# Optimization experiments

Hardware: AMD Instinct MI355X
Metric: run time of the kernel (lower is better)

The kernel has to match this reference:

```python
import jax, jax.numpy as jnp
import numpy as np

B, T_ENC, E, T_DEC, N_MELS, H, A = 32, 256, 512, 200, 80, 1024, 128


def setup_inputs() -> dict:
    key = jax.random.key(0)
    ks = jax.random.split(key, 20)
    rn = lambda k, s, sc: (jax.random.normal(k, s, jnp.float32) * sc)
    return {
        "inputs": rn(ks[0], (B, T_ENC, E), 1.0),
        "padded_mels": rn(ks[1], (B, N_MELS, T_DEC), 1.0),
        "W_enc": rn(ks[2], (E, A), 0.04),
        "W_q": rn(ks[3], (H, A), 0.03),
        "conv_w": rn(ks[4], (32, 1, 31), 0.18),
        "conv_b": jnp.zeros((32,), jnp.float32),
        "W_loc": rn(ks[5], (32, A), 0.18),
        "v_e": rn(ks[6], (A,), 0.09),
        "pw1": rn(ks[7], (N_MELS, 256), 0.11),
        "pb1": jnp.zeros((256,), jnp.float32),
        "pw2": rn(ks[8], (256, 256), 0.06),
        "pb2": jnp.zeros((256,), jnp.float32),
        "Wi1": rn(ks[9], (256 + E, 4 * H), 0.03),
        "Wh1": rn(ks[10], (H, 4 * H), 0.03),
        "bl1": jnp.zeros((4 * H,), jnp.float32),
        "Wi2": rn(ks[11], (H, 4 * H), 0.03),
        "Wh2": rn(ks[12], (H, 4 * H), 0.03),
        "bl2": jnp.zeros((4 * H,), jnp.float32),
        "Wp": rn(ks[13], (H + E, N_MELS), 0.025),
        "bp": jnp.zeros((N_MELS,), jnp.float32),
    }


def _lstm_cell(x, h, c, Wi, Wh, b):
    g = x @ Wi + h @ Wh + b
    i, f, gg, o = jnp.split(g, 4, axis=-1)
    c = jax.nn.sigmoid(f) * c + jax.nn.sigmoid(i) * jnp.tanh(gg)
    h = jax.nn.sigmoid(o) * jnp.tanh(c)
    return h, c


def reference(inputs, padded_mels, W_enc, W_q, conv_w, conv_b, W_loc, v_e,
              pw1, pb1, pw2, pb2, Wi1, Wh1, bl1, Wi2, Wh2, bl2, Wp, bp):
    b, t_enc, e = inputs.shape
    n_mels, t_dec = padded_mels.shape[1], padded_mels.shape[2]
    proc_enc = inputs @ W_enc  # [B, T_enc, A]
    # teacher forcing: prepend go frame, use frames 0..T_dec-1 as inputs
    go = jnp.zeros((b, n_mels, 1), inputs.dtype)
    prev_mels = jnp.moveaxis(jnp.concatenate([go, padded_mels], axis=-1)[:, :, :-1], -1, 0)  # [T_dec,B,80]

    def step(carry, prev_mel):
        h1, c1, h2, c2, ctx, aw_cum = carry
        # prenet (dropout omitted: eval/deterministic reference)
        x = jax.nn.relu(prev_mel @ pw1 + pb1)
        x = jax.nn.relu(x @ pw2 + pb2)
        # 2-layer LSTM on [prenet, prev context]
        lstm_in = jnp.concatenate([x, ctx], axis=-1)
        h1n, c1n = _lstm_cell(lstm_in, h1, c1, Wi1, Wh1, bl1)
        h2n, c2n = _lstm_cell(h1n, h2, c2, Wi2, Wh2, bl2)
        # location-sensitive attention
        q = h2n @ W_q  # [B, A]
        loc = jax.lax.conv_general_dilated(aw_cum[:, None, :], conv_w, (1,), "SAME",
                                           dimension_numbers=("NCH", "OIH", "NCH"))
        loc = loc + conv_b[None, :, None]
        loc = jnp.swapaxes(loc, 1, 2) @ W_loc  # [B, T_enc, A]
        energies = jnp.tanh(q[:, None, :] + loc + proc_enc) @ v_e  # [B, T_enc]
        aw = jax.nn.softmax(energies, axis=1)
        ctx_n = jnp.einsum("bt,bte->be", aw, inputs)
        out = jnp.concatenate([h2n, ctx_n], axis=-1) @ Wp + bp  # [B, 80]
        return (h1n, c1n, h2n, c2n, ctx_n, aw_cum + aw), out

    z = lambda *s: jnp.zeros(s, inputs.dtype)
    carry0 = (z(b, H), z(b, H), z(b, H), z(b, H), z(b, e), z(b, t_enc))
    _, mels = jax.lax.scan(step, carry0, prev_mels)
    return mels  # [T_dec, B, 80]
```

## Files before the change

kernel.cpp:

```cpp
#include <hip/hip_runtime.h>
#include <hip/hip_fp16.h>

#define BB   32
#define TENC 256
#define EE   512
#define TDEC 200
#define NM   80
#define HH   1024
#define AA   128
#define GG   4096
#define K1   1792
#define K2   2048

typedef _Float16 h8v  __attribute__((ext_vector_type(8)));
typedef float    f32x4 __attribute__((ext_vector_type(4)));

__device__ __forceinline__ float sigf(float x){ return 1.0f/(1.0f + __expf(-x)); }
__device__ __forceinline__ float tanhfast(float x){ return 1.0f - 2.0f/(1.0f + __expf(2.0f*x)); }


__global__ void k_zero(float* __restrict__ p, int n){
    int i = blockIdx.x*blockDim.x + threadIdx.x;
    if(i < n) p[i] = 0.f;
}

__global__ void k_cvt_half(const float* __restrict__ src, __half* __restrict__ dst, int n){
    int i = blockIdx.x*blockDim.x + threadIdx.x;
    int stride = gridDim.x*blockDim.x;
    for(; i<n; i+=stride) dst[i] = __float2half(src[i]);
}

__global__ __launch_bounds__(256) void k_transpose2(const float* __restrict__ src,
                                                    _Float16* __restrict__ dst,
                                                    int K, int C, int dstStride, int kOff, int pack){
    __shared__ float tile[32][33];
    const int tid = threadIdx.x;
    const int c0 = blockIdx.x*32, k0 = blockIdx.y*32;
    const int cl = tid & 31, r8 = tid >> 5;
    #pragma unroll
    for(int i=0;i<4;i++){
        const int k = k0 + r8 + i*8;
        if(k < K && c0+cl < C) tile[r8 + i*8][cl] = src[(size_t)k*C + c0 + cl];
    }
    __syncthreads();
    const int kl = tid & 31, c8 = tid >> 5;
    #pragma unroll
    for(int i=0;i<4;i++){
        const int c = c0 + c8 + i*8;
        if(c < C && k0+kl < K){
            const int p = pack ? ((c & 1023)*4 + (c >> 10)) : c;
            dst[(size_t)p*dstStride + kOff + k0 + kl] = (_Float16)tile[kl][c8 + i*8];
        }
    }
}

__global__ __launch_bounds__(256) void k_wfrag(const _Float16* __restrict__ WT,
                                               _Float16* __restrict__ WF, int K){
    const int tid = threadIdx.x;
    const int l = tid & 63, f = tid >> 6;
    const int ct = blockIdx.y;
    const int kc = blockIdx.x*4 + f;
    const h8v v = *(const h8v*)(WT + (size_t)(ct*16 + (l & 15))*K + kc*32 + ((l >> 4) << 3));
    *(h8v*)(WF + ((size_t)(ct*(K >> 5) + kc)*64 + l)*8) = v;
}

__global__ __launch_bounds__(128) void k_proc_enc(const float* __restrict__ inputs,
                                                  const float* __restrict__ Wenc,
                                                  __half* __restrict__ pe_h){
    const int row = blockIdx.x;
    const int a   = threadIdx.x;
    const float* in = inputs + (size_t)row*EE;
    float acc = 0.f;
    for(int k=0;k<EE;k++) acc = fmaf(in[k], Wenc[k*AA + a], acc);
    pe_h[(size_t)row*AA + a] = __float2half(acc);
}

__global__ __launch_bounds__(320) void k_pip(const float* __restrict__ inputs,
                                             const float* __restrict__ Wp_c,
                                             __half* __restrict__ PIP){
    const int b = blockIdx.x >> 6, t4 = (blockIdx.x & 63)*4;
    __shared__ float xs[4*EE];
    const int tid = threadIdx.x;
    for(int i=tid; i<4*EE; i+=320) xs[i] = inputs[((size_t)b*TENC + t4)*EE + i];
    __syncthreads();
    const int tl = tid/80, m = tid%80;
    float acc = 0.f;
    for(int k=0;k<EE;k++) acc = fmaf(xs[tl*EE + k], Wp_c[k*NM + m], acc);
    PIP[((size_t)b*TENC + t4 + tl)*NM + m] = __float2half(acc);
}

__global__ __launch_bounds__(256) void k_prenet(const float* __restrict__ pmels,
                                                const float* __restrict__ pw1, const float* __restrict__ pb1,
                                                const float* __restrict__ pw2, const float* __restrict__ pb2,
                                                _Float16* __restrict__ XS1h){
    const int t = blockIdx.x;
    __shared__ float pm[BB*NM];
    __shared__ float h1s[BB*256];
    const int tid = threadIdx.x;
    for(int el=tid; el<BB*NM; el+=256){
        const int b = el/NM, m = el%NM;
        pm[el] = (t==0) ? 0.f : pmels[(size_t)(b*NM + m)*TDEC + (t-1)];
    }
    __syncthreads();
    const int a = tid;
    float acc[BB];
    #pragma unroll
    for(int b=0;b<BB;b++) acc[b]=0.f;
    for(int m=0;m<NM;m++){
        const float w = pw1[m*256 + a];
        #pragma unroll
        for(int b=0;b<BB;b++) acc[b] = fmaf(pm[b*NM+m], w, acc[b]);
    }
    {
        const float bias = pb1[a];
        for(int b=0;b<BB;b++) h1s[b*256+a] = fmaxf(acc[b]+bias, 0.f);
    }
    __syncthreads();
    #pragma unroll
    for(int b=0;b<BB;b++) acc[b]=0.f;
    for(int k=0;k<256;k++){
        const float w = pw2[k*256 + a];
        #pragma unroll
        for(int b=0;b<BB;b++) acc[b] = fmaf(h1s[b*256+k], w, acc[b]);
    }
    {
        const float bias = pb2[a];
        #pragma unroll
        for(int b=0;b<BB;b++)
            XS1h[((size_t)t*BB + b)*K1 + a] = (_Float16)fmaxf(acc[b]+bias, 0.f);
    }
}

__global__ void k_mloc(const float* __restrict__ conv_w, const float* __restrict__ conv_b,
                       const float* __restrict__ W_loc, float* __restrict__ Mloc, float* __restrict__ cbp){
    const int a = threadIdx.x;
    for(int d=0; d<31; d++){
        float s = 0.f;
        for(int ch=0; ch<32; ch++) s = fmaf(conv_w[ch*31 + d], W_loc[ch*AA + a], s);
        Mloc[d*AA + a] = s;
    }
    float s = 0.f;
    for(int ch=0; ch<32; ch++) s = fmaf(conv_b[ch], W_loc[ch*AA + a], s);
    cbp[a] = s;
}


template<int K>
__global__ __launch_bounds__(512) void k_lstm_mfma(
    const _Float16* __restrict__ XSh, const _Float16* __restrict__ WF,
    const float* __restrict__ bias, float* __restrict__ cst,
    _Float16* __restrict__ hA, int strideA, int offA,
    _Float16* __restrict__ hB, int strideB, int offB,
    float* __restrict__ hF)
{
    constexpr int KCN = K/128;
    __shared__ float part[4*32*18];
    const int tid = threadIdx.x, bid = blockIdx.x;
    const int l = tid & 63, w = tid >> 6;
    const int kw = w & 3, mh = w >> 2;

    f32x4 acc0 = {0.f,0.f,0.f,0.f}, acc1 = {0.f,0.f,0.f,0.f};
    const int row = mh*16 + (l & 15);
    const _Float16* aptr = XSh + (size_t)row*K + kw*(K/4) + ((l >> 4) << 3);
    const _Float16* bptr = WF + ((size_t)(bid*(K >> 5) + kw*KCN)*64 + l)*8;
    #pragma unroll
    for(int kc=0; kc<KCN; kc+=2){
        const h8v a0 = *(const h8v*)(aptr + (size_t)kc*32);
        const h8v b0 = *(const h8v*)(bptr + (size_t)kc*512);
        const h8v a1 = *(const h8v*)(aptr + (size_t)(kc+1)*32);
        const h8v b1 = *(const h8v*)(bptr + (size_t)(kc+1)*512);
        acc0 = __builtin_amdgcn_mfma_f32_16x16x32_f16(a0, b0, acc0, 0, 0, 0);
        acc1 = __builtin_amdgcn_mfma_f32_16x16x32_f16(a1, b1, acc1, 0, 0, 0);
    }
    {
        const int r0 = mh*16 + ((l >> 4) << 2);
        const int c  = l & 15;
        #pragma unroll
        for(int j=0;j<4;j++)
            part[(kw*32 + r0 + j)*18 + c] = acc0[j] + acc1[j];
    }
    __syncthreads();
    if(tid < 128){
        const int b = tid & 31, cl = tid >> 5;
        float g[4];
        #pragma unroll
        for(int gi=0; gi<4; gi++){
            const int c = cl*4 + gi;
            float s = part[(0*32 + b)*18 + c] + part[(1*32 + b)*18 + c]
                    + part[(2*32 + b)*18 + c] + part[(3*32 + b)*18 + c];
            const int p = bid*16 + c;
            g[gi] = s + bias[(p & 3)*HH + (p >> 2)];
        }
        const int cell = bid*4 + cl;
        const int ci = cell*BB + b;
        const float cn = sigf(g[1])*cst[ci] + sigf(g[0])*tanhfast(g[2]);
        cst[ci] = cn;
        const float hv = sigf(g[3])*tanhfast(cn);
        hA[(size_t)b*strideA + offA + cell] = (_Float16)hv;
        if(hB) hB[(size_t)b*strideB + offB + cell] = (_Float16)hv;
        if(hF) hF[(size_t)b*HH + cell] = hv;
    }
}

__global__ __launch_bounds__(256) void k_qe(
    const float* __restrict__ h2f,
    const _Float16* __restrict__ WqT, const float* __restrict__ cbp,
    const float* __restrict__ Mloc, const float* __restrict__ ve,
    const float* __restrict__ awc, const __half* __restrict__ pe,
    float* __restrict__ e_ws)
{
    const int b = blockIdx.x >> 3, ts = blockIdx.x & 7;
    const int t0 = ts*32;
    const int tid = threadIdx.x;
    __shared__ float h2s[1024], qc[256], qf[128], ml[31*AA], ves[AA], awin[64], ep[256];
    for(int i=tid; i<1024; i+=256) h2s[i] = h2f[(size_t)b*HH + i];
    for(int i=tid; i<31*AA; i+=256) ml[i] = Mloc[i];
    if(tid < AA) ves[tid] = ve[tid];
    if(tid < 62){
        const int g = t0 - 15 + tid;
        awin[tid] = (g>=0 && g<TENC) ? awc[b*TENC+g] : 0.f;
    }
    __syncthreads();
    {
        const int a = tid & 127, tp = tid >> 7;
        float qa = 0.f;
        const _Float16* wq = WqT + (size_t)a*HH + tp*512;
        const float* hs = h2s + tp*512;
        for(int kb=0; kb<512; kb+=8){
            const h8v w8 = *(const h8v*)(wq + kb);
            #pragma unroll
            for(int i2=0;i2<8;i2++) qa = fmaf((float)w8[i2], hs[kb+i2], qa);
        }
        qc[tp*AA + a] = qa;
    }
    __syncthreads();
    if(tid < AA) qf[tid] = qc[tid] + qc[AA+tid] + cbp[tid];
    __syncthreads();
    {
        const int tl = tid & 31, aq = tid >> 5;
        const int a0 = aq*16;
        const int t  = t0 + tl;
        float s[16];
        const __half* pp = pe + ((size_t)(b*TENC + t))*AA + a0;
        #pragma unroll
        for(int j=0;j<16;j++) s[j] = qf[a0+j] + __half2float(pp[j]);
        for(int d=0;d<31;d++){
            const float w = awin[tl+d];
            #pragma unroll
            for(int j=0;j<16;j++) s[j] = fmaf(w, ml[d*AA + a0 + j], s[j]);
        }
        float es = 0.f;
        #pragma unroll
        for(int j=0;j<16;j++) es = fmaf(tanhfast(s[j]), ves[a0+j], es);
        ep[aq*32 + tl] = es;
    }
    __syncthreads();
    if(tid < 32){
        float e = 0.f;
        #pragma unroll
        for(int q=0;q<8;q++) e += ep[q*32 + tid];
        e_ws[b*TENC + t0 + tid] = e;
    }
}

__global__ __launch_bounds__(256) void k_attn(
    const float* __restrict__ e_ws, const __half* __restrict__ inputs_h,
    const __half* __restrict__ PIP, float* __restrict__ awc,
    _Float16* __restrict__ XS1hn,
    const float* __restrict__ h2f,
    const _Float16* __restrict__ WohT, const float* __restrict__ bp,
    float* __restrict__ out, int t)
{
    const int b = blockIdx.x, tid = threadIdx.x;
    __shared__ float aw[TENC], h2s[1024], red[320], sred[8];
    for(int i=tid; i<1024; i+=256) h2s[i] = h2f[(size_t)b*HH + i];
    const float e = e_ws[b*TENC + tid];
    float m = e;
    #pragma unroll
    for(int o=32;o>=1;o>>=1) m = fmaxf(m, __shfl_xor(m, o));
    if((tid&63)==0) sred[tid>>6] = m;
    __syncthreads();
    m = fmaxf(fmaxf(sred[0],sred[1]), fmaxf(sred[2],sred[3]));
    const float p = __expf(e - m);
    float sum = p;
    #pragma unroll
    for(int o=32;o>=1;o>>=1) sum += __shfl_xor(sum, o);
    if((tid&63)==0) sred[4+(tid>>6)] = sum;
    __syncthreads();
    sum = sred[4]+sred[5]+sred[6]+sred[7];
    const float awv = p/sum;
    aw[tid] = awv;
    awc[b*TENC + tid] += awv;
    __syncthreads();
    {
        float a0=0.f, a1=0.f;
        const __half* ib = inputs_h + (size_t)b*TENC*EE;
        for(int tt=0; tt<TENC; tt+=4){
            const float4 w4 = *(const float4*)&aw[tt];
            a0 = fmaf(w4.x, __half2float(ib[(size_t)(tt+0)*EE + tid]),       a0);
            a1 = fmaf(w4.x, __half2float(ib[(size_t)(tt+0)*EE + 256 + tid]), a1);
            a0 = fmaf(w4.y, __half2float(ib[(size_t)(tt+1)*EE + tid]),       a0);
            a1 = fmaf(w4.y, __half2float(ib[(size_t)(tt+1)*EE + 256 + tid]), a1);
            a0 = fmaf(w4.z, __half2float(ib[(size_t)(tt+2)*EE + tid]),       a0);
            a1 = fmaf(w4.z, __half2float(ib[(size_t)(tt+2)*EE + 256 + tid]), a1);
            a0 = fmaf(w4.w, __half2float(ib[(size_t)(tt+3)*EE + tid]),       a0);
            a1 = fmaf(w4.w, __half2float(ib[(size_t)(tt+3)*EE + 256 + tid]), a1);
        }
        _Float16* xrow = XS1hn + (size_t)b*K1 + 256;
        xrow[tid]       = (_Float16)a0;
        xrow[256 + tid] = (_Float16)a1;
    }
    if(tid < 160){
        const int m2 = tid % 80, kh = tid / 80;
        float s1 = 0.f;
        const _Float16* wo = WohT + (size_t)m2*HH + kh*512;
        const float* hs = h2s + kh*512;
        for(int kb=0; kb<512; kb+=8){
            const h8v w8 = *(const h8v*)(wo + kb);
            #pragma unroll
            for(int i2=0;i2<8;i2++) s1 = fmaf((float)w8[i2], hs[kb+i2], s1);
        }
        red[kh*80 + m2] = s1;
        float s2 = 0.f;
        const __half* pp = PIP + ((size_t)(b*TENC) + kh*128)*NM + m2;
        const float* awp = aw + kh*128;
        for(int tt=0; tt<128; tt++) s2 = fmaf(awp[tt], __half2float(pp[(size_t)tt*NM]), s2);
        red[160 + kh*80 + m2] = s2;
    }
    __syncthreads();
    if(tid < NM){
        const float o = red[tid] + red[80+tid] + red[160+tid] + red[240+tid] + bp[tid];
        out[((size_t)t*BB + b)*NM + tid] = o;
    }
}


extern "C" void kernel_launch(void* const* d_in, const int* in_sizes, int n_in,
                              void* d_out, int out_size, void* d_ws, size_t ws_size,
                              hipStream_t stream)
{
    const float* inputs = (const float*)d_in[0];
    const float* pmels  = (const float*)d_in[1];
    const float* W_enc  = (const float*)d_in[2];
    const float* W_q    = (const float*)d_in[3];
    const float* conv_w = (const float*)d_in[4];
    const float* conv_b = (const float*)d_in[5];
    const float* W_loc  = (const float*)d_in[6];
    const float* v_e    = (const float*)d_in[7];
    const float* pw1    = (const float*)d_in[8];
    const float* pb1    = (const float*)d_in[9];
    const float* pw2    = (const float*)d_in[10];
    const float* pb2    = (const float*)d_in[11];
    const float* Wi1    = (const float*)d_in[12];
    const float* Wh1    = (const float*)d_in[13];
    const float* bl1    = (const float*)d_in[14];
    const float* Wi2    = (const float*)d_in[15];
    const float* Wh2    = (const float*)d_in[16];
    const float* bl2    = (const float*)d_in[17];
    const float* Wp     = (const float*)d_in[18];
    const float* bp     = (const float*)d_in[19];
    float* out = (float*)d_out;
    (void)in_sizes; (void)n_in; (void)out_size; (void)ws_size;

    char* ws = (char*)d_ws;
    size_t off = 0;
    auto carve = [&](size_t bytes)->char* {
        char* p = ws + off;
        off += (bytes + 255) & ~(size_t)255;
        return p;
    };
    __half*    inputs_h = (__half*)   carve((size_t)BB*TENC*EE*2);
    __half*    pe_h     = (__half*)   carve((size_t)BB*TENC*AA*2);
    __half*    PIP      = (__half*)   carve((size_t)BB*TENC*NM*2);
    _Float16*  XS1h     = (_Float16*) carve((size_t)(TDEC+1)*BB*K1*2);
    _Float16*  XS2h     = (_Float16*) carve((size_t)2*BB*K2*2);
    _Float16*  WA       = (_Float16*) carve((size_t)GG*K2*2);
    _Float16*  WB       = (_Float16*) carve((size_t)GG*K1*2);
    _Float16*  W2F      = (_Float16*) carve((size_t)GG*K2*2);
    _Float16*  WqT      = (_Float16*) carve((size_t)AA*HH*2);
    _Float16*  WohT     = (_Float16*) carve((size_t)NM*HH*2);
    const int NZ = HH*BB + HH*BB + BB*TENC;
    float* zblk = (float*)carve((size_t)NZ*4);
    float* c1  = zblk;
    float* c2  = c1 + HH*BB;
    float* awc = c2 + HH*BB;
    float* h2f  = (float*)carve((size_t)BB*HH*4);
    float* e_ws = (float*)carve((size_t)BB*TENC*4);
    float* Mloc = (float*)carve((size_t)31*AA*4);
    float* cbp  = (float*)carve((size_t)AA*4);
    _Float16* W1F = WA;

    k_zero<<<(NZ+255)/256,256,0,stream>>>(zblk, NZ);
    k_zero<<<(2*BB*K2/2+255)/256,256,0,stream>>>((float*)XS2h, 2*BB*K2/2);
    k_zero<<<(BB*K1/2+255)/256,256,0,stream>>>((float*)XS1h, BB*K1/2);
    k_cvt_half<<<2048,256,0,stream>>>(inputs, inputs_h, BB*TENC*EE);
    k_proc_enc<<<BB*TENC,128,0,stream>>>(inputs, W_enc, pe_h);
    k_prenet<<<TDEC,256,0,stream>>>(pmels, pw1,pb1,pw2,pb2, XS1h);
    k_mloc<<<1,128,0,stream>>>(conv_w, conv_b, W_loc, Mloc, cbp);
    k_transpose2<<<dim3(GG/32, 1024/32),256,0,stream>>>(Wi2, WA, 1024, GG, K2, 0,    1);
    k_transpose2<<<dim3(GG/32, 1024/32),256,0,stream>>>(Wh2, WA, 1024, GG, K2, 1024, 1);
    k_wfrag<<<dim3(K2/128, GG/16),256,0,stream>>>(WA, W2F, K2);
    k_transpose2<<<dim3(GG/32,  768/32),256,0,stream>>>(Wi1, WB, 768,  GG, K1, 0,    1);
    k_transpose2<<<dim3(GG/32, 1024/32),256,0,stream>>>(Wh1, WB, 1024, GG, K1, 768,  1);
    k_wfrag<<<dim3(K1/128, GG/16),256,0,stream>>>(WB, W1F, K1);
    k_transpose2<<<dim3(AA/32, 1024/32),256,0,stream>>>(W_q, WqT, 1024, AA, HH, 0,   0);
    k_transpose2<<<dim3(3,     1024/32),256,0,stream>>>(Wp,  WohT, 1024, NM, HH, 0,  0);
    k_pip<<<BB*64,320,0,stream>>>(inputs, Wp + (size_t)HH*NM, PIP);

    for(int t=0; t<TDEC; t++){
        const int p = t & 1;
        _Float16* x1c = XS1h + (size_t)t*BB*K1;
        _Float16* x1n = XS1h + (size_t)(t+1)*BB*K1;
        _Float16* x2p = XS2h + (size_t)p*BB*K2;
        _Float16* x2n = XS2h + (size_t)(1-p)*BB*K2;

        k_lstm_mfma<K1><<<256,512,0,stream>>>(x1c, W1F, bl1, c1,
                                              x2p, K2, 0,
                                              x1n, K1, 768,
                                              (float*)nullptr);
        k_lstm_mfma<K2><<<256,512,0,stream>>>(x2p, W2F, bl2, c2,
                                              x2n, K2, 1024,
                                              (_Float16*)nullptr, 0, 0,
                                              h2f);
        k_qe<<<256,256,0,stream>>>(h2f, WqT, cbp, Mloc, v_e, awc, pe_h, e_ws);
        k_attn<<<BB,256,0,stream>>>(e_ws, inputs_h, PIP, awc, x1n, h2f,
                                    WohT, bp, out, t);
    }
}
```

Baseline: 11.19 ms.

## Fuse per-step decoder kernels into one persistent cooperative kernel with grid syncs

Replaces the four kernel launches per decoder step (two LSTM layers, energy, attention/output) with a single cooperative kernel of 256 blocks that loops over all 200 steps and separates phases with grid-wide syncs. The LSTM phase is restructured so each of the 8 waves covers a K-slice for both batch halves, sharing each weight fragment load across two MFMAs. Attention and output work are re-split for 512-thread blocks. This removes roughly 800 launch overheads, at the cost of grid barrier latency and idle blocks during the attention phase, which only 32 blocks execute.

```diff
diff --git a/kernel.cpp b/kernel.cpp
--- a/kernel.cpp
+++ b/kernel.cpp
@@ -1,5 +1,8 @@
 #include <hip/hip_runtime.h>
 #include <hip/hip_fp16.h>
+#include <hip/hip_cooperative_groups.h>
+
+namespace cg = cooperative_groups;
 
 #define BB   32
 #define TENC 256
@@ -146,38 +149,34 @@
 
 
 template<int K>
-__global__ __launch_bounds__(512) void k_lstm_mfma(
+__device__ __forceinline__ void lstm_phase(
     const _Float16* __restrict__ XSh, const _Float16* __restrict__ WF,
     const float* __restrict__ bias, float* __restrict__ cst,
-    _Float16* __restrict__ hA, int strideA, int offA,
-    _Float16* __restrict__ hB, int strideB, int offB,
-    float* __restrict__ hF)
+    _Float16* hA, int strideA, int offA,
+    _Float16* hB, int strideB, int offB,
+    float* hF, float* part, int tid, int bid)
 {
-    constexpr int KCN = K/128;
-    __shared__ float part[4*32*18];
-    const int tid = threadIdx.x, bid = blockIdx.x;
-    const int l = tid & 63, w = tid >> 6;
-    const int kw = w & 3, mh = w >> 2;
-
-    f32x4 acc0 = {0.f,0.f,0.f,0.f}, acc1 = {0.f,0.f,0.f,0.f};
-    const int row = mh*16 + (l & 15);
-    const _Float16* aptr = XSh + (size_t)row*K + kw*(K/4) + ((l >> 4) << 3);
+    constexpr int KCN = K/256;
+    const int l = tid & 63, kw = tid >> 6;
+    f32x4 accL = {0.f,0.f,0.f,0.f}, accH = {0.f,0.f,0.f,0.f};
+    const int r = l & 15;
+    const _Float16* aptr = XSh + (size_t)r*K + kw*KCN*32 + ((l >> 4) << 3);
     const _Float16* bptr = WF + ((size_t)(bid*(K >> 5) + kw*KCN)*64 + l)*8;
     #pragma unroll
-    for(int kc=0; kc<KCN; kc+=2){
-        const h8v a0 = *(const h8v*)(aptr + (size_t)kc*32);
-        const h8v b0 = *(const h8v*)(bptr + (size_t)kc*512);
-        const h8v a1 = *(const h8v*)(aptr + (size_t)(kc+1)*32);
-        const h8v b1 = *(const h8v*)(bptr + (size_t)(kc+1)*512);
-        acc0 = __builtin_amdgcn_mfma_f32_16x16x32_f16(a0, b0, acc0, 0, 0, 0);
-        acc1 = __builtin_amdgcn_mfma_f32_16x16x32_f16(a1, b1, acc1, 0, 0, 0);
+    for(int kc=0; kc<KCN; kc++){
+        const h8v b8 = *(const h8v*)(bptr + (size_t)kc*512);
+        const h8v aL = *(const h8v*)(aptr + (size_t)kc*32);
+        const h8v aH = *(const h8v*)(aptr + (size_t)16*K + kc*32);
+        accL = __builtin_amdgcn_mfma_f32_16x16x32_f16(aL, b8, accL, 0, 0, 0);
+        accH = __builtin_amdgcn_mfma_f32_16x16x32_f16(aH, b8, accH, 0, 0, 0);
     }
     {
-        const int r0 = mh*16 + ((l >> 4) << 2);
-        const int c  = l & 15;
+        const int r0 = (l >> 4) << 2, c = l & 15;
         #pragma unroll
-        for(int j=0;j<4;j++)
-            part[(kw*32 + r0 + j)*18 + c] = acc0[j] + acc1[j];
+        for(int j=0;j<4;j++){
+            part[(kw*32 + r0 + j)*18 + c]      = accL[j];
+            part[(kw*32 + 16 + r0 + j)*18 + c] = accH[j];
+        }
     }
     __syncthreads();
     if(tid < 128){
@@ -185,10 +184,11 @@
         float g[4];
         #pragma unroll
         for(int gi=0; gi<4; gi++){
-            const int c = cl*4 + gi;
-            float s = part[(0*32 + b)*18 + c] + part[(1*32 + b)*18 + c]
-                    + part[(2*32 + b)*18 + c] + part[(3*32 + b)*18 + c];
-            const int p = bid*16 + c;
+            const int c2 = cl*4 + gi;
+            float s = 0.f;
+            #pragma unroll
+            for(int q=0;q<8;q++) s += part[(q*32 + b)*18 + c2];
+            const int p = bid*16 + c2;
             g[gi] = s + bias[(p & 3)*HH + (p >> 2)];
         }
         const int cell = bid*4 + cl;
@@ -202,135 +202,182 @@
     }
 }
 
-__global__ __launch_bounds__(256) void k_qe(
-    const float* __restrict__ h2f,
+__global__ __launch_bounds__(512) void k_decode(
+    _Float16* __restrict__ XS1h, _Float16* __restrict__ XS2h,
+    const _Float16* __restrict__ W1F, const _Float16* __restrict__ W2F,
+    const float* __restrict__ bl1, const float* __restrict__ bl2,
+    float* __restrict__ c1, float* __restrict__ c2,
     const _Float16* __restrict__ WqT, const float* __restrict__ cbp,
     const float* __restrict__ Mloc, const float* __restrict__ ve,
-    const float* __restrict__ awc, const __half* __restrict__ pe,
-    float* __restrict__ e_ws)
+    float* __restrict__ awc, const __half* __restrict__ pe,
+    float* __restrict__ e_ws,
+    const __half* __restrict__ inputs_h, const __half* __restrict__ PIP,
+    const _Float16* __restrict__ WohT, const float* __restrict__ bp,
+    float* __restrict__ h2f, float* __restrict__ out)
 {
-    const int b = blockIdx.x >> 3, ts = blockIdx.x & 7;
-    const int t0 = ts*32;
-    const int tid = threadIdx.x;
-    __shared__ float h2s[1024], qc[256], qf[128], ml[31*AA], ves[AA], awin[64], ep[256];
-    for(int i=tid; i<1024; i+=256) h2s[i] = h2f[(size_t)b*HH + i];
-    for(int i=tid; i<31*AA; i+=256) ml[i] = Mloc[i];
-    if(tid < AA) ves[tid] = ve[tid];
-    if(tid < 62){
-        const int g = t0 - 15 + tid;
-        awin[tid] = (g>=0 && g<TENC) ? awc[b*TENC+g] : 0.f;
-    }
-    __syncthreads();
-    {
-        const int a = tid & 127, tp = tid >> 7;
-        float qa = 0.f;
-        const _Float16* wq = WqT + (size_t)a*HH + tp*512;
-        const float* hs = h2s + tp*512;
-        for(int kb=0; kb<512; kb+=8){
-            const h8v w8 = *(const h8v*)(wq + kb);
+    cg::grid_group gg = cg::this_grid();
+    const int tid = threadIdx.x, bid = blockIdx.x;
+
+    __shared__ float s_ml[31*AA];
+    __shared__ float s_ves[AA];
+    __shared__ float s_part[8*32*18];
+    __shared__ float s_h2s[1024];
+    __shared__ float s_qc[4*AA];
+    __shared__ float s_qf[AA];
+    __shared__ float s_awin[64];
+    __shared__ float s_ep[16*32];
+    __shared__ float s_aw[TENC];
+    __shared__ float s_red1[320];
+    __shared__ float s_red2[320];
+    __shared__ float s_sred[8];
+
+    for(int i=tid; i<31*AA; i+=512) s_ml[i] = Mloc[i];
+    if(tid < AA) s_ves[tid] = ve[tid];
+    __syncthreads();
+
+    for(int t=0; t<TDEC; t++){
+        const int p = t & 1;
+        const _Float16* x1c = XS1h + (size_t)t*BB*K1;
+        _Float16* x1n = XS1h + (size_t)(t+1)*BB*K1;
+        _Float16* x2p = XS2h + (size_t)p*BB*K2;
+        _Float16* x2n = XS2h + (size_t)(1-p)*BB*K2;
+
+        lstm_phase<K1>(x1c, W1F, bl1, c1,
+                       x2p, K2, 0,
+                       x1n, K1, 768,
+                       (float*)nullptr, s_part, tid, bid);
+        gg.sync();
+
+        lstm_phase<K2>(x2p, W2F, bl2, c2,
+                       x2n, K2, 1024,
+                       (_Float16*)nullptr, 0, 0,
+                       h2f, s_part, tid, bid);
+        gg.sync();
+
+        {
+            const int b = bid >> 3, ts = bid & 7;
+            const int t0 = ts*32;
+            for(int i=tid; i<1024; i+=512) s_h2s[i] = h2f[(size_t)b*HH + i];
+            if(tid < 62){
+                const int g = t0 - 15 + tid;
+                s_awin[tid] = (g>=0 && g<TENC) ? awc[b*TENC+g] : 0.f;
+            }
+            __syncthreads();
+            {
+                const int a = tid & 127, tp = tid >> 7;
+                float qa = 0.f;
+                const _Float16* wq = WqT + (size_t)a*HH + tp*256;
+                const float* hs = s_h2s + tp*256;
+                for(int kb=0; kb<256; kb+=8){
+                    const h8v w8 = *(const h8v*)(wq + kb);
+                    #pragma unroll
+                    for(int i2=0;i2<8;i2++) qa = fmaf((float)w8[i2], hs[kb+i2], qa);
+                }
+                s_qc[tp*AA + a] = qa;
+            }
+            __syncthreads();
+            if(tid < AA) s_qf[tid] = s_qc[tid] + s_qc[AA+tid] + s_qc[2*AA+tid] + s_qc[3*AA+tid] + cbp[tid];
+            __syncthreads();
+            {
+                const int tl = tid & 31, aq = tid >> 5;
+                const int a0 = aq*8;
+                const int tt = t0 + tl;
+                float s[8];
+                const __half* pp = pe + ((size_t)(b*TENC + tt))*AA + a0;
+                #pragma unroll
+                for(int j=0;j<8;j++) s[j] = s_qf[a0+j] + __half2float(pp[j]);
+                for(int d=0;d<31;d++){
+                    const float w = s_awin[tl+d];
+                    #pragma unroll
+                    for(int j=0;j<8;j++) s[j] = fmaf(w, s_ml[d*AA + a0 + j], s[j]);
+                }
+                float es = 0.f;
+                #pragma unroll
+                for(int j=0;j<8;j++) es = fmaf(tanhfast(s[j]), s_ves[a0+j], es);
+                s_ep[aq*32 + tl] = es;
+            }
+            __syncthreads();
+            if(tid < 32){
+                float e = 0.f;
+                #pragma unroll
+                for(int q=0;q<16;q++) e += s_ep[q*32 + tid];
+                e_ws[b*TENC + t0 + tid] = e;
+            }
+        }
+        gg.sync();
+
+        if(bid < BB){
+            const int b = bid;
+            float* ctxred = s_part;
+            for(int i=tid; i<1024; i+=512) s_h2s[i] = h2f[(size_t)b*HH + i];
+            float e = -1e30f;
+            if(tid < 256) e = e_ws[b*TENC + tid];
+            float m = e;
             #pragma unroll
-            for(int i2=0;i2<8;i2++) qa = fmaf((float)w8[i2], hs[kb+i2], qa);
+            for(int o=32;o>=1;o>>=1) m = fmaxf(m, __shfl_xor(m, o));
+            if((tid&63)==0 && tid<256) s_sred[tid>>6] = m;
+            __syncthreads();
+            m = fmaxf(fmaxf(s_sred[0],s_sred[1]), fmaxf(s_sred[2],s_sred[3]));
+            const float pv = (tid<256) ? __expf(e - m) : 0.f;
+            float sum = pv;
+            #pragma unroll
+            for(int o=32;o>=1;o>>=1) sum += __shfl_xor(sum, o);
+            if((tid&63)==0 && tid<256) s_sred[4+(tid>>6)] = sum;
+            __syncthreads();
+            sum = s_sred[4]+s_sred[5]+s_sred[6]+s_sred[7];
+            if(tid < 256){
+                const float awv = pv/sum;
+                s_aw[tid] = awv;
+                awc[b*TENC + tid] += awv;
+            }
+            __syncthreads();
+            {
+                const int ch8 = tid & 63, tq = tid >> 6;
+                const __half* ib = inputs_h + (size_t)b*TENC*EE + ch8*8;
+                float a_[8];
+                #pragma unroll
+                for(int j=0;j<8;j++) a_[j]=0.f;
+                for(int tt=tq; tt<TENC; tt+=8){
+                    const float wv = s_aw[tt];
+                    const h8v x8 = *(const h8v*)(ib + (size_t)tt*EE);
+                    #pragma unroll
+                    for(int j=0;j<8;j++) a_[j] = fmaf(wv, (float)x8[j], a_[j]);
+                }
+                #pragma unroll
+                for(int j=0;j<8;j++) ctxred[tq*512 + ch8*8 + j] = a_[j];
+            }
+            __syncthreads();
+            {
+                float s = 0.f;
+                #pragma unroll
+                for(int q=0;q<8;q++) s += ctxred[q*512 + tid];
+                x1n[(size_t)b*K1 + 256 + tid] = (_Float16)s;
+            }
+            if(tid < 320){
+                const int m2 = tid % 80, kh = tid / 80;
+                float s1 = 0.f;
+                const _Float16* wo = WohT + (size_t)m2*HH + kh*256;
+                const float* hs = s_h2s + kh*256;
+                for(int kb=0; kb<256; kb+=8){
+                    const h8v w8 = *(const h8v*)(wo + kb);
+                    #pragma unroll
+                    for(int i2=0;i2<8;i2++) s1 = fmaf((float)w8[i2], hs[kb+i2], s1);
+                }
+                s_red1[kh*80 + m2] = s1;
+                float s2 = 0.f;
+                const __half* pp = PIP + ((size_t)(b*TENC) + kh*64)*NM + m2;
+                const float* awp = s_aw + kh*64;
+                for(int tt=0; tt<64; tt++) s2 = fmaf(awp[tt], __half2float(pp[(size_t)tt*NM]), s2);
+                s_red2[kh*80 + m2] = s2;
+            }
+            __syncthreads();
+            if(tid < NM){
+                const float o = s_red1[tid]+s_red1[80+tid]+s_red1[160+tid]+s_red1[240+tid]
+                              + s_red2[tid]+s_red2[80+tid]+s_red2[160+tid]+s_red2[240+tid] + bp[tid];
+                out[((size_t)t*BB + b)*NM + tid] = o;
+            }
         }
-        qc[tp*AA + a] = qa;
-    }
-    __syncthreads();
-    if(tid < AA) qf[tid] = qc[tid] + qc[AA+tid] + cbp[tid];
-    __syncthreads();
-    {
-        const int tl = tid & 31, aq = tid >> 5;
-        const int a0 = aq*16;
-        const int t  = t0 + tl;
-        float s[16];
-        const __half* pp = pe + ((size_t)(b*TENC + t))*AA + a0;
-        #pragma unroll
-        for(int j=0;j<16;j++) s[j] = qf[a0+j] + __half2float(pp[j]);
-        for(int d=0;d<31;d++){
-            const float w = awin[tl+d];
-            #pragma unroll
-            for(int j=0;j<16;j++) s[j] = fmaf(w, ml[d*AA + a0 + j], s[j]);
-        }
-        float es = 0.f;
-        #pragma unroll
-        for(int j=0;j<16;j++) es = fmaf(tanhfast(s[j]), ves[a0+j], es);
-        ep[aq*32 + tl] = es;
-    }
-    __syncthreads();
-    if(tid < 32){
-        float e = 0.f;
-        #pragma unroll
-        for(int q=0;q<8;q++) e += ep[q*32 + tid];
-        e_ws[b*TENC + t0 + tid] = e;
-    }
-}
-
-__global__ __launch_bounds__(256) void k_attn(
-    const float* __restrict__ e_ws, const __half* __restrict__ inputs_h,
-    const __half* __restrict__ PIP, float* __restrict__ awc,
-    _Float16* __restrict__ XS1hn,
-    const float* __restrict__ h2f,
-    const _Float16* __restrict__ WohT, const float* __restrict__ bp,
-    float* __restrict__ out, int t)
-{
-    const int b = blockIdx.x, tid = threadIdx.x;
-    __shared__ float aw[TENC], h2s[1024], red[320], sred[8];
-    for(int i=tid; i<1024; i+=256) h2s[i] = h2f[(size_t)b*HH + i];
-    const float e = e_ws[b*TENC + tid];
-    float m = e;
-    #pragma unroll
-    for(int o=32;o>=1;o>>=1) m = fmaxf(m, __shfl_xor(m, o));
-    if((tid&63)==0) sred[tid>>6] = m;
-    __syncthreads();
-    m = fmaxf(fmaxf(sred[0],sred[1]), fmaxf(sred[2],sred[3]));
-    const float p = __expf(e - m);
-    float sum = p;
-    #pragma unroll
-    for(int o=32;o>=1;o>>=1) sum += __shfl_xor(sum, o);
-    if((tid&63)==0) sred[4+(tid>>6)] = sum;
-    __syncthreads();
-    sum = sred[4]+sred[5]+sred[6]+sred[7];
-    const float awv = p/sum;
-    aw[tid] = awv;
-    awc[b*TENC + tid] += awv;
-    __syncthreads();
-    {
-        float a0=0.f, a1=0.f;
-        const __half* ib = inputs_h + (size_t)b*TENC*EE;
-        for(int tt=0; tt<TENC; tt+=4){
-            const float4 w4 = *(const float4*)&aw[tt];
-            a0 = fmaf(w4.x, __half2float(ib[(size_t)(tt+0)*EE + tid]),       a0);
-            a1 = fmaf(w4.x, __half2float(ib[(size_t)(tt+0)*EE + 256 + tid]), a1);
-            a0 = fmaf(w4.y, __half2float(ib[(size_t)(tt+1)*EE + tid]),       a0);
-            a1 = fmaf(w4.y, __half2float(ib[(size_t)(tt+1)*EE + 256 + tid]), a1);
-            a0 = fmaf(w4.z, __half2float(ib[(size_t)(tt+2)*EE + tid]),       a0);
-            a1 = fmaf(w4.z, __half2float(ib[(size_t)(tt+2)*EE + 256 + tid]), a1);
-            a0 = fmaf(w4.w, __half2float(ib[(size_t)(tt+3)*EE + tid]),       a0);
-            a1 = fmaf(w4.w, __half2float(ib[(size_t)(tt+3)*EE + 256 + tid]), a1);
-        }
-        _Float16* xrow = XS1hn + (size_t)b*K1 + 256;
-        xrow[tid]       = (_Float16)a0;
-        xrow[256 + tid] = (_Float16)a1;
-    }
-    if(tid < 160){
-        const int m2 = tid % 80, kh = tid / 80;
-        float s1 = 0.f;
-        const _Float16* wo = WohT + (size_t)m2*HH + kh*512;
-        const float* hs = h2s + kh*512;
-        for(int kb=0; kb<512; kb+=8){
-            const h8v w8 = *(const h8v*)(wo + kb);
-            #pragma unroll
-            for(int i2=0;i2<8;i2++) s1 = fmaf((float)w8[i2], hs[kb+i2], s1);
-        }
-        red[kh*80 + m2] = s1;
-        float s2 = 0.f;
-        const __half* pp = PIP + ((size_t)(b*TENC) + kh*128)*NM + m2;
-        const float* awp = aw + kh*128;
-        for(int tt=0; tt<128; tt++) s2 = fmaf(awp[tt], __half2float(pp[(size_t)tt*NM]), s2);
-        red[160 + kh*80 + m2] = s2;
-    }
-    __syncthreads();
-    if(tid < NM){
-        const float o = red[tid] + red[80+tid] + red[160+tid] + red[240+tid] + bp[tid];
-        out[((size_t)t*BB + b)*NM + tid] = o;
+        gg.sync();
     }
 }
 
@@ -407,23 +454,30 @@
     k_transpose2<<<dim3(3,     1024/32),256,0,stream>>>(Wp,  WohT, 1024, NM, HH, 0,  0);
     k_pip<<<BB*64,320,0,stream>>>(inputs, Wp + (size_t)HH*NM, PIP);
 
-    for(int t=0; t<TDEC; t++){
-        const int p = t & 1;
-        _Float16* x1c = XS1h + (size_t)t*BB*K1;
-        _Float16* x1n = XS1h + (size_t)(t+1)*BB*K1;
-        _Float16* x2p = XS2h + (size_t)p*BB*K2;
-        _Float16* x2n = XS2h + (size_t)(1-p)*BB*K2;
-
-        k_lstm_mfma<K1><<<256,512,0,stream>>>(x1c, W1F, bl1, c1,
-                                              x2p, K2, 0,
-                                              x1n, K1, 768,
-                                              (float*)nullptr);
-        k_lstm_mfma<K2><<<256,512,0,stream>>>(x2p, W2F, bl2, c2,
-                                              x2n, K2, 1024,
-                                              (_Float16*)nullptr, 0, 0,
-                                              h2f);
-        k_qe<<<256,256,0,stream>>>(h2f, WqT, cbp, Mloc, v_e, awc, pe_h, e_ws);
-        k_attn<<<BB,256,0,stream>>>(e_ws, inputs_h, PIP, awc, x1n, h2f,
-                                    WohT, bp, out, t);
-    }
-}
+    {
+        void* ka[21];
+        ka[0]  = (void*)&XS1h;
+        ka[1]  = (void*)&XS2h;
+        ka[2]  = (void*)&W1F;
+        ka[3]  = (void*)&W2F;
+        ka[4]  = (void*)&bl1;
+        ka[5]  = (void*)&bl2;
+        ka[6]  = (void*)&c1;
+        ka[7]  = (void*)&c2;
+        ka[8]  = (void*)&WqT;
+        ka[9]  = (void*)&cbp;
+        ka[10] = (void*)&Mloc;
+        ka[11] = (void*)&v_e;
+        ka[12] = (void*)&awc;
+        ka[13] = (void*)&pe_h;
+        ka[14] = (void*)&e_ws;
+        ka[15] = (void*)&inputs_h;
+        ka[16] = (void*)&PIP;
+        ka[17] = (void*)&WohT;
+        ka[18] = (void*)&bp;
+        ka[19] = (void*)&h2f;
+        ka[20] = (void*)&out;
+        hipLaunchCooperativeKernel((const void*)k_decode, dim3(256), dim3(512),
+                                   ka, 0, stream);
+    }
+}
```

Measured after the change: 43.86 ms. +291.8%, slower.
